# Kernel optimization log

Measured on AMD Instinct MI355X. Metric: run time of the kernel, lower is better.

The kernel has to match this reference:

```python
import jax, jax.numpy as jnp
import numpy as np

N, E, F, HID, HEADS, L, B, R = 50000, 400000, 64, 256, 4, 4, 16, 8
C = HID // HEADS  # per-head channels = 64
LN_EPS = 1e-5
NEG_SLOPE = 0.2  # GATConv LeakyReLU default


def _posenc(n, d):
    pos = jnp.arange(n, dtype=jnp.float32)[:, None]
    i = jnp.arange(d, dtype=jnp.float32)[None, :]
    rates = 1.0 / 10000.0 ** (2.0 * jnp.floor(i / 2.0) / d)
    ang = pos * rates
    return jnp.where(jnp.arange(d)[None, :] % 2 == 0, jnp.sin(ang), jnp.cos(ang))


def _layernorm(x, g, b):
    mu = x.mean(-1, keepdims=True)
    var = ((x - mu) ** 2).mean(-1, keepdims=True)
    return (x - mu) * jax.lax.rsqrt(var + LN_EPS) * g + b


def _gat_layer(x, src, dst, W, a_src, a_dst, bias):
    # x: [N, HID]; W: [HID, HID]; a_src/a_dst: [HEADS, C]; bias: [HID]
    h = (x @ W).reshape(N, HEADS, C)
    s_src = (h * a_src[None]).sum(-1)  # [N, HEADS]
    s_dst = (h * a_dst[None]).sum(-1)  # [N, HEADS]
    e = jax.nn.leaky_relu(s_src[src] + s_dst[dst], NEG_SLOPE)  # [E', HEADS]
    m = jax.ops.segment_max(e, dst, num_segments=N)
    ex = jnp.exp(e - m[dst])
    denom = jax.ops.segment_sum(ex, dst, num_segments=N)
    alpha = ex / denom[dst]  # softmax over incoming edges per dst node
    out = jax.ops.segment_sum(alpha[:, :, None] * h[src], dst, num_segments=N)
    return out.reshape(N, HID) + bias


def setup_inputs() -> dict:
    key = jax.random.key(0)
    ks = jax.random.split(key, 20)
    sc = 0.05
    batch = jnp.sort(jax.random.randint(ks[2], (N,), 0, B))
    return {
        "x": jax.random.normal(ks[0], (N, F), jnp.float32),
        "region_emb_w": jax.random.normal(ks[3], (R, F), jnp.float32) * sc,
        "in_proj_w": jax.random.normal(ks[4], (3 * F, HID), jnp.float32) * sc,
        "in_proj_b": jnp.zeros((HID,), jnp.float32),
        "gat_w": jax.random.normal(ks[5], (L, HID, HID), jnp.float32) * sc,
        "att_src": jax.random.normal(ks[6], (L, HEADS, C), jnp.float32) * sc,
        "att_dst": jax.random.normal(ks[7], (L, HEADS, C), jnp.float32) * sc,
        "gat_b": jnp.zeros((L, HID), jnp.float32),
        "ln_g": jnp.ones((L, HID), jnp.float32),
        "ln_b": jnp.zeros((L, HID), jnp.float32),
        "ro_w1": jax.random.normal(ks[8], (HID, HID), jnp.float32) * sc,
        "ro_b1": jnp.zeros((HID,), jnp.float32),
        "ro_w2": jax.random.normal(ks[9], (HID, HID), jnp.float32) * sc,
        "ro_b2": jnp.zeros((HID,), jnp.float32),
        "edge_index": jax.random.randint(ks[1], (2, E), 0, N),
        "batch": batch,
        "region_ids": jax.random.randint(ks[10], (N,), 0, R),
    }


def reference(x, region_emb_w, in_proj_w, in_proj_b, gat_w, att_src, att_dst,
              gat_b, ln_g, ln_b, ro_w1, ro_b1, ro_w2, ro_b2,
              edge_index, batch, region_ids):
    # input features: x | region embedding | sinusoidal posenc  -> [N, 3F]
    feats = jnp.concatenate([x, region_emb_w[region_ids], _posenc(N, F)], axis=-1)
    h = feats @ in_proj_w + in_proj_b
    # add self loops once (GATConv add_self_loops=True)
    loop = jnp.arange(N)
    src = jnp.concatenate([edge_index[0], loop])
    dst = jnp.concatenate([edge_index[1], loop])
    for l in range(L):
        h = _gat_layer(h, src, dst, gat_w[l], att_src[l], att_dst[l], gat_b[l])
        h = _layernorm(jax.nn.relu(h), ln_g[l], ln_b[l])
        # dropout is identity in eval mode
    # global mean pool over graphs
    sums = jax.ops.segment_sum(h, batch, num_segments=B)
    cnts = jax.ops.segment_sum(jnp.ones((N,), h.dtype), batch, num_segments=B)
    pooled = sums / jnp.maximum(cnts, 1.0)[:, None]  # [B, HID]
    out = jax.nn.gelu(pooled @ ro_w1 + ro_b1, approximate=False) @ ro_w2 + ro_b2
    return out
```

## Files before the change

### kernel.cpp

```cpp
#include <hip/hip_runtime.h>
#include <cmath>

typedef unsigned short u16;
typedef unsigned char u8;
typedef unsigned int u32;
typedef short bf16x8 __attribute__((ext_vector_type(8)));
typedef float f32x4 __attribute__((ext_vector_type(4)));
typedef float f32x2 __attribute__((ext_vector_type(2)));

#define NN 50000
#define MP 50048
#define EE 400000
#define ET 450000
#define HIDD 256
#define KIN 192
#define LN_EPSF 1e-5f

__device__ __forceinline__ float bf2f(u16 u){ return __uint_as_float(((u32)u)<<16); }
__device__ __forceinline__ u16 f2bf(float f){
  u32 x = __float_as_uint(f);
  u32 r = x + 0x7fffu + ((x>>16)&1u);
  return (u16)(r>>16);
}
__device__ __forceinline__ u32 pack2(float a, float b){ return (u32)f2bf(a) | ((u32)f2bf(b)<<16); }
__device__ __forceinline__ u8 f2fp8(float v){
  return (u8)(__builtin_amdgcn_cvt_pk_fp8_f32(v, v, 0, false) & 0xff);
}

__device__ __forceinline__ void dma16(const u16* g, u16* lds){
  __builtin_amdgcn_global_load_lds(
      (const __attribute__((address_space(1))) void*)g,
      (__attribute__((address_space(3))) void*)lds, 16, 0, 0);
}

__global__ __launch_bounds__(256) void k_setup(
    const float* __restrict__ x, const float* __restrict__ remb, const int* __restrict__ rid,
    u16* __restrict__ feats,
    const float* __restrict__ ipw, const float* __restrict__ gatw,
    u16* __restrict__ wtin, u16* __restrict__ wtl,
    const float* __restrict__ asrc, const float* __restrict__ adst, u16* __restrict__ vmat,
    const int* __restrict__ ei, int* __restrict__ deg)
{
  int b = blockIdx.x;
  if (b < 1564){
    int u = b*256 + threadIdx.x;
    int n = u >> 3;
    int c0 = (u & 7) * 8;
    uint4 o = {0u,0u,0u,0u};
    if (n < NN){
      const float* xp = x + (size_t)n*64 + c0;
      float4 v0 = *(const float4*)xp;
      float4 v1 = *(const float4*)(xp + 4);
      o.x = pack2(v0.x, v0.y); o.y = pack2(v0.z, v0.w);
      o.z = pack2(v1.x, v1.y); o.w = pack2(v1.z, v1.w);
    }
    *(uint4*)(feats + (size_t)n*192 + c0) = o;
  } else if (b < 3128){
    int u = (b-1564)*256 + threadIdx.x;
    int n = u >> 3;
    int c0 = (u & 7) * 8;
    uint4 o = {0u,0u,0u,0u};
    if (n < NN){
      const float* rp = remb + (size_t)rid[n]*64 + c0;
      float4 v0 = *(const float4*)rp;
      float4 v1 = *(const float4*)(rp + 4);
      o.x = pack2(v0.x, v0.y); o.y = pack2(v0.z, v0.w);
      o.z = pack2(v1.x, v1.y); o.w = pack2(v1.z, v1.w);
    }
    *(uint4*)(feats + (size_t)n*192 + 64 + c0) = o;
  } else if (b < 4692){
    int u = (b-3128)*256 + threadIdx.x;
    int n = u >> 3;
    int i0 = (u & 7) * 8;
    uint4 o = {0u,0u,0u,0u};
    if (n < NN){
      float fn = (float)n;
      float os[8];
      #pragma unroll
      for (int m=0;m<4;++m){
        float rate = exp2f(-(float)(i0 + 2*m) * (1.0f/64.0f) * 13.287712379549449f);
        float s, c;
        __sincosf(fn * rate, &s, &c);
        os[2*m] = s; os[2*m+1] = c;
      }
      o.x = pack2(os[0], os[1]); o.y = pack2(os[2], os[3]);
      o.z = pack2(os[4], os[5]); o.w = pack2(os[6], os[7]);
    }
    *(uint4*)(feats + (size_t)n*192 + 128 + i0) = o;
  } else if (b < 5908){
    int idx = (b - 4692)*256 + threadIdx.x;
    if (idx < 49152){
      int n = idx / 192, k = idx - n*192;
      wtin[idx] = f2bf(ipw[k*256 + n]);
    } else {
      int j = idx - 49152;
      if (j < 262144){
        int l = j >> 16, rem = j & 65535;
        int n = rem >> 8, k = rem & 255;
        wtl[j] = f2bf(gatw[l*65536 + k*256 + n]);
      }
    }
  } else if (b < 5972){
    int idx = (b - 5908)*256 + threadIdx.x;
    if (idx < 16384){
      int l = idx >> 12, rem = idx & 4095, v = rem >> 8, k = rem & 255;
      float s = 0.f;
      if (v < 8){
        const float* a = (v < 4) ? (asrc + l*256 + v*64) : (adst + l*256 + (v-4)*64);
        const float* w = gatw + (size_t)l*65536 + k*256 + (v & 3)*64;
        #pragma unroll 8
        for (int c=0;c<64;++c) s += w[c]*a[c];
      }
      vmat[idx] = f2bf(s);
    }
  } else {
    int i = (b - 5972)*256 + threadIdx.x;
    if (i < ET){
      int d = (i < EE) ? ei[EE + i] : (i - EE);
      atomicAdd(&deg[d], 1);
    }
  }
}

__global__ void k_scan1(const int* __restrict__ deg, int* __restrict__ row_off, int* __restrict__ part){
  __shared__ int s[256];
  int n = blockIdx.x*256 + threadIdx.x;
  int v = (n < NN) ? deg[n] : 0;
  s[threadIdx.x] = v;
  __syncthreads();
  for (int off=1; off<256; off<<=1){
    int t = (threadIdx.x >= off) ? s[threadIdx.x - off] : 0;
    __syncthreads();
    s[threadIdx.x] += t;
    __syncthreads();
  }
  if (n < NN) row_off[n] = s[threadIdx.x] - v;
  if (threadIdx.x == 255) part[blockIdx.x] = s[255];
}

__global__ void k_scan23(int* __restrict__ row_off, const int* __restrict__ part, int nparts){
  __shared__ int sp[256];
  int t = threadIdx.x;
  sp[t] = (t < nparts && t < (int)blockIdx.x) ? part[t] : 0;
  __syncthreads();
  for (int off=128; off; off>>=1){
    if (t < off) sp[t] += sp[t+off];
    __syncthreads();
  }
  int n = blockIdx.x*256 + t;
  if (n < NN) row_off[n] += sp[0];
}

__global__ void k_scatter(const int* __restrict__ ei, const int* __restrict__ row_off,
                          int* __restrict__ cur, int* __restrict__ csr_src){
  int i = blockIdx.x*blockDim.x + threadIdx.x;
  if (i >= ET) return;
  int s, d;
  if (i < EE){ s = ei[i]; d = ei[EE + i]; } else { s = i - EE; d = i - EE; }
  int pos = row_off[d] + atomicAdd(&cur[d], 1);
  csr_src[pos] = s;
}

template<int K>
__global__ __launch_bounds__(256, 3) void k_gemm(
    const u16* __restrict__ A, const u16* __restrict__ Wt,
    const float* __restrict__ bias, const u16* __restrict__ vmat,
    float* __restrict__ ss, float* __restrict__ sd,
    u16* __restrict__ C, u8* __restrict__ C8, int M)
{
  __shared__ u16 Asl[2][128*32];
  __shared__ u16 Bsl[2][128*32];
  int tid = threadIdx.x;
  int wave = tid >> 6, lane = tid & 63, quad = lane >> 4, lm = lane & 15;

  int bid0 = blockIdx.x;
  int xcd = bid0 & 7, off = bid0 >> 3;
  const int q = 782 >> 3, r = 782 & 7;
  int wgid = (xcd < r ? xcd*(q+1) : r*(q+1) + (xcd - r)*q) + off;
  int r0 = (wgid >> 1) * 128;
  int cb = wgid & 1;

  int rW = (wave >> 1) * 64;
  int cW = (wave & 1) * 64;
  bool doScore = vmat && (cb == 0) && ((wave & 1) == 0);

  f32x4 acc[4][4] = {};
  f32x4 accs[4] = {};

  auto stage = [&](int buf, int k0){
    for (int m = wave; m < 8; m += 4){
      int s = m*64 + lane;
      int rr = s >> 2, p = s & 3;
      int c = p ^ ((rr >> 2) & 3);
      dma16(A + (size_t)(r0 + rr)*K + k0 + c*8, &Asl[buf][m*512]);
    }
    for (int m = wave; m < 8; m += 4){
      int s = m*64 + lane;
      int rr = s >> 2, p = s & 3;
      int c = p ^ ((rr >> 2) & 3);
      dma16(Wt + (size_t)(cb*128 + rr)*K + k0 + c*8, &Bsl[buf][m*512]);
    }
  };

  stage(0, 0);
  __syncthreads();

  for (int ks = 0; ks < K/32; ++ks){
    int cur = ks & 1;
    if (ks + 1 < K/32) stage(cur ^ 1, (ks+1)*32);

    bf16x8 a[4], b[4];
    #pragma unroll
    for (int i=0;i<4;++i){
      int row = rW + i*16 + lm;
      int slot = row*4 + (quad ^ ((row >> 2) & 3));
      a[i] = *(const bf16x8*)(&Asl[cur][slot*8]);
    }
    #pragma unroll
    for (int j=0;j<4;++j){
      int row = cW + j*16 + lm;
      int slot = row*4 + (quad ^ ((row >> 2) & 3));
      b[j] = *(const bf16x8*)(&Bsl[cur][slot*8]);
    }
    #pragma unroll
    for (int i=0;i<4;++i)
      #pragma unroll
      for (int j=0;j<4;++j)
        acc[i][j] = __builtin_amdgcn_mfma_f32_16x16x32_bf16(a[i], b[j], acc[i][j], 0, 0, 0);
    if (doScore){
      bf16x8 bs = *(const bf16x8*)(vmat + (size_t)lm*K + ks*32 + quad*8);
      #pragma unroll
      for (int i=0;i<4;++i)
        accs[i] = __builtin_amdgcn_mfma_f32_16x16x32_bf16(a[i], bs, accs[i], 0, 0, 0);
    }
    __syncthreads();
  }

  if (doScore){
    #pragma unroll
    for (int i=0;i<4;++i){
      #pragma unroll
      for (int r2=0;r2<4;++r2){
        int row = r0 + rW + i*16 + quad*4 + r2;
        if (row < M){
          if (lm < 4)      ss[row*4 + lm]     = accs[i][r2];
          else if (lm < 8) sd[row*4 + lm - 4] = accs[i][r2];
        }
      }
    }
  }

  #pragma unroll
  for (int i=0;i<4;++i){
    #pragma unroll
    for (int r2=0;r2<4;++r2){
      int row = r0 + rW + i*16 + quad*4 + r2;
      if (row < M){
        #pragma unroll
        for (int j=0;j<4;++j){
          int col = cb*128 + cW + j*16 + lm;
          float v = acc[i][j][r2];
          if (bias) v += bias[col];
          if (C)  C[(size_t)row*256 + col] = f2bf(v);
          if (C8) C8[(size_t)row*256 + col] = f2fp8(v);
        }
      }
    }
  }
}

__global__ __launch_bounds__(256) void k_aggregate(
    const u8* __restrict__ h8, const float* __restrict__ ssrc, const float* __restrict__ sdst,
    const int* __restrict__ row_off, const int* __restrict__ deg, const int* __restrict__ csr_src,
    const float* __restrict__ bias, const float* __restrict__ g, const float* __restrict__ bb,
    u16* __restrict__ hout, u8* __restrict__ hout8)
{
  int wv = (blockIdx.x*blockDim.x + threadIdx.x) >> 6;
  int lane = threadIdx.x & 63;
  int half = lane >> 5;
  int hl = lane & 31;
  int n = wv*2 + half;
  if (n >= NN) return;
  int c0 = hl*8;
  int head = hl >> 3;
  float sdh = sdst[n*4 + head];
  int ro = row_off[n];
  int dg = deg[n];
  float denA = 0.f, denB = 0.f;
  float a0=0,a1=0,a2=0,a3=0,a4=0,a5=0,a6=0,a7=0;
  float b0=0,b1=0,b2=0,b3=0,b4=0,b5=0,b6=0,b7=0;

  int sA = csr_src[ro];
  int sB = (1 < dg) ? csr_src[ro + 1] : 0;
  uint2 uA = *(const uint2*)(h8 + (size_t)sA*HIDD + c0);
  uint2 uB = *(const uint2*)(h8 + (size_t)sB*HIDD + c0);
  float fA = ssrc[sA*4 + head];
  float fB = ssrc[sB*4 + head];

  for (int j = 0; j < dg; j += 2){
    bool hasB = (j + 1 < dg);
    int nA = (j + 2 < dg) ? csr_src[ro + j + 2] : 0;
    int nB = (j + 3 < dg) ? csr_src[ro + j + 3] : 0;
    uint2 vA = *(const uint2*)(h8 + (size_t)nA*HIDD + c0);
    uint2 vB = *(const uint2*)(h8 + (size_t)nB*HIDD + c0);
    float gA = ssrc[nA*4 + head];
    float gB = ssrc[nB*4 + head];

    float eA = fA + sdh;
    eA = (eA > 0.f) ? eA : 0.2f*eA;
    float xA = __expf(eA);
    denA += xA;
    f32x2 pA0 = __builtin_amdgcn_cvt_pk_f32_fp8((int)uA.x, false);
    f32x2 pA1 = __builtin_amdgcn_cvt_pk_f32_fp8((int)uA.x, true);
    f32x2 pA2 = __builtin_amdgcn_cvt_pk_f32_fp8((int)uA.y, false);
    f32x2 pA3 = __builtin_amdgcn_cvt_pk_f32_fp8((int)uA.y, true);
    a0 += xA*pA0.x; a1 += xA*pA0.y; a2 += xA*pA1.x; a3 += xA*pA1.y;
    a4 += xA*pA2.x; a5 += xA*pA2.y; a6 += xA*pA3.x; a7 += xA*pA3.y;
    if (hasB){
      float eB = fB + sdh;
      eB = (eB > 0.f) ? eB : 0.2f*eB;
      float xB = __expf(eB);
      denB += xB;
      f32x2 pB0 = __builtin_amdgcn_cvt_pk_f32_fp8((int)uB.x, false);
      f32x2 pB1 = __builtin_amdgcn_cvt_pk_f32_fp8((int)uB.x, true);
      f32x2 pB2 = __builtin_amdgcn_cvt_pk_f32_fp8((int)uB.y, false);
      f32x2 pB3 = __builtin_amdgcn_cvt_pk_f32_fp8((int)uB.y, true);
      b0 += xB*pB0.x; b1 += xB*pB0.y; b2 += xB*pB1.x; b3 += xB*pB1.y;
      b4 += xB*pB2.x; b5 += xB*pB2.y; b6 += xB*pB3.x; b7 += xB*pB3.y;
    }
    sA = nA; sB = nB; uA = vA; uB = vB; fA = gA; fB = gB;
  }

  float inv = 1.f / (denA + denB);
  float y[8];
  y[0]=a0+b0; y[1]=a1+b1; y[2]=a2+b2; y[3]=a3+b3;
  y[4]=a4+b4; y[5]=a5+b5; y[6]=a6+b6; y[7]=a7+b7;
  float4 bi0 = *(const float4*)(bias + c0);
  float4 bi1 = *(const float4*)(bias + c0 + 4);
  y[0]=fmaxf(y[0]*inv+bi0.x,0.f); y[1]=fmaxf(y[1]*inv+bi0.y,0.f);
  y[2]=fmaxf(y[2]*inv+bi0.z,0.f); y[3]=fmaxf(y[3]*inv+bi0.w,0.f);
  y[4]=fmaxf(y[4]*inv+bi1.x,0.f); y[5]=fmaxf(y[5]*inv+bi1.y,0.f);
  y[6]=fmaxf(y[6]*inv+bi1.z,0.f); y[7]=fmaxf(y[7]*inv+bi1.w,0.f);
  float sum = (y[0]+y[1])+(y[2]+y[3])+((y[4]+y[5])+(y[6]+y[7]));
  #pragma unroll
  for (int o=16;o>=1;o>>=1) sum += __shfl_xor(sum, o);
  float mu = sum * (1.f/256.f);
  float d[8], sq = 0.f;
  #pragma unroll
  for (int k=0;k<8;++k){ d[k] = y[k]-mu; sq += d[k]*d[k]; }
  #pragma unroll
  for (int o=16;o>=1;o>>=1) sq += __shfl_xor(sq, o);
  float rs = rsqrtf(sq*(1.f/256.f) + LN_EPSF);
  float4 g0 = *(const float4*)(g + c0);
  float4 g1 = *(const float4*)(g + c0 + 4);
  float4 q0 = *(const float4*)(bb + c0);
  float4 q1 = *(const float4*)(bb + c0 + 4);
  float o0 = d[0]*rs*g0.x + q0.x, o1 = d[1]*rs*g0.y + q0.y;
  float o2 = d[2]*rs*g0.z + q0.z, o3 = d[3]*rs*g0.w + q0.w;
  float o4v= d[4]*rs*g1.x + q1.x, o5 = d[5]*rs*g1.y + q1.y;
  float o6 = d[6]*rs*g1.z + q1.z, o7 = d[7]*rs*g1.w + q1.w;
  if (hout8){
    u32 w0 = (u32)__builtin_amdgcn_cvt_pk_fp8_f32(o0, o1, 0, false);
    w0 = (u32)__builtin_amdgcn_cvt_pk_fp8_f32(o2, o3, (int)w0, true);
    u32 w1 = (u32)__builtin_amdgcn_cvt_pk_fp8_f32(o4v, o5, 0, false);
    w1 = (u32)__builtin_amdgcn_cvt_pk_fp8_f32(o6, o7, (int)w1, true);
    uint2 o8; o8.x = w0; o8.y = w1;
    *(uint2*)(hout8 + (size_t)n*HIDD + c0) = o8;
  } else {
    uint4 o4;
    o4.x = pack2(o0, o1);
    o4.y = pack2(o2, o3);
    o4.z = pack2(o4v, o5);
    o4.w = pack2(o6, o7);
    *(uint4*)(hout + (size_t)n*HIDD + c0) = o4;
  }
}

__global__ __launch_bounds__(256) void k_pool(
    const u8* __restrict__ h8, const int* __restrict__ batch,
    float* __restrict__ pooled, float* __restrict__ cnt)
{
  const int chunk = 50;
  int t = threadIdx.x;
  int n0 = blockIdx.x*chunk;
  int n1 = min(n0 + chunk, NN);
  if (n0 >= n1) return;
  float acc = 0.f;
  int curb = batch[n0];
  int runStart = n0;
  bool hi = (t & 2) != 0;
  for (int n=n0; n<n1; ++n){
    int b = batch[n];
    if (b != curb){
      atomicAdd(&pooled[curb*HIDD + t], acc);
      if (t == 0) atomicAdd(&cnt[curb], (float)(n - runStart));
      acc = 0.f; curb = b; runStart = n;
    }
    u32 w = *(const u32*)(h8 + (size_t)n*HIDD + (t & ~3));
    f32x2 p = hi ? __builtin_amdgcn_cvt_pk_f32_fp8((int)w, true)
                 : __builtin_amdgcn_cvt_pk_f32_fp8((int)w, false);
    acc += (t & 1) ? p.y : p.x;
  }
  atomicAdd(&pooled[curb*HIDD + t], acc);
  if (t == 0) atomicAdd(&cnt[curb], (float)(n1 - runStart));
}

__global__ __launch_bounds__(256) void k_readout(
    const float* __restrict__ pooled, const float* __restrict__ cnt,
    const float* __restrict__ w1, const float* __restrict__ b1,
    const float* __restrict__ w2, const float* __restrict__ b2,
    float* __restrict__ out)
{
  __shared__ float p[256], mid[256];
  int b = blockIdx.x, t = threadIdx.x;
  float c = fmaxf(cnt[b], 1.f);
  p[t] = pooled[b*HIDD + t] / c;
  __syncthreads();
  float acc = b1[t];
  for (int k=0;k<256;++k) acc += p[k]*w1[k*256+t];
  mid[t] = 0.5f*acc*(1.f + erff(acc*0.70710678118654752f));
  __syncthreads();
  float acc2 = b2[t];
  for (int k=0;k<256;++k) acc2 += mid[k]*w2[k*256+t];
  out[b*HIDD + t] = acc2;
}

extern "C" void kernel_launch(void* const* d_in, const int* in_sizes, int n_in,
                              void* d_out, int out_size, void* d_ws, size_t ws_size,
                              hipStream_t stream)
{
  const float* x    = (const float*)d_in[0];
  const float* remb = (const float*)d_in[1];
  const float* ipw  = (const float*)d_in[2];
  const float* ipb  = (const float*)d_in[3];
  const float* gatw = (const float*)d_in[4];
  const float* asrc = (const float*)d_in[5];
  const float* adst = (const float*)d_in[6];
  const float* gatb = (const float*)d_in[7];
  const float* lng  = (const float*)d_in[8];
  const float* lnb  = (const float*)d_in[9];
  const float* row1 = (const float*)d_in[10];
  const float* rob1 = (const float*)d_in[11];
  const float* row2 = (const float*)d_in[12];
  const float* rob2 = (const float*)d_in[13];
  const int* ei   = (const int*)d_in[14];
  const int* batch= (const int*)d_in[15];
  const int* rid  = (const int*)d_in[16];

  char* ws = (char*)d_ws;
  int*   deg  = (int*)  (ws + 0);
  int*   cur  = (int*)  (ws + 200192);
  float* cnt  = (float*)(ws + 400384);
  float* pool = (float*)(ws + 400640);
  int*   row  = (int*)  (ws + 417024);
  int*   part = (int*)  (ws + 617216);
  int*   csr  = (int*)  (ws + 618240);
  float* ss   = (float*)(ws + 2418432);
  float* sd   = (float*)(ws + 3219200);
  u16*   vmat = (u16*)  (ws + 4019968);
  u16*   feats= (u16*)  (ws + 4052736);
  u16*   wtin = (u16*)  (ws + 23271168);
  u16*   wtl  = (u16*)  (ws + 23369472);
  u16*   hA   = (u16*)  (ws + 23893760);
  u8*    hA8  = (u8*)   (ws + 23893760);
  u8*    hB8  = (u8*)   (ws + 49518336);

  (void)hipMemsetAsync(ws, 0, 417024, stream);

  k_setup <<<7730, 256, 0, stream>>>(x, remb, rid, feats, ipw, gatw, wtin, wtl,
                                     asrc, adst, vmat, ei, deg);
  k_scan1 <<<196, 256, 0, stream>>>(deg, row, part);
  k_scan23<<<196, 256, 0, stream>>>(row, part, 196);
  k_scatter<<<1758, 256, 0, stream>>>(ei, row, cur, csr);

  k_gemm<KIN><<<782, 256, 0, stream>>>(feats, wtin, ipb, nullptr,
                                       nullptr, nullptr, hA, nullptr, NN);

  for (int l = 0; l < 4; ++l){
    k_gemm<HIDD><<<782, 256, 0, stream>>>(hA, wtl + (size_t)l*HIDD*HIDD, nullptr,
                                          vmat + (size_t)l*16*256, ss, sd,
                                          nullptr, hB8, NN);
    if (l < 3){
      k_aggregate<<<6250, 256, 0, stream>>>(hB8, ss, sd, row, deg, csr,
                                            gatb + l*HIDD, lng + l*HIDD, lnb + l*HIDD,
                                            hA, nullptr);
    } else {
      k_aggregate<<<6250, 256, 0, stream>>>(hB8, ss, sd, row, deg, csr,
                                            gatb + l*HIDD, lng + l*HIDD, lnb + l*HIDD,
                                            nullptr, hA8);
    }
  }

  k_pool   <<<1000, 256, 0, stream>>>(hA8, batch, pool, cnt);
  k_readout<<<16, 256, 0, stream>>>(pool, cnt, row1, rob1, row2, rob2, (float*)d_out);
}
```

Baseline: 452.9 us.

## Fold input projection into first GAT layer weight, dropping one GEMM pass

Precomputes the product of the input projection weight and the first GAT layer weight, plus the folded bias and attention-score vectors, inside the setup kernel. The first layer then runs a single K=192 GEMM straight from the raw features to the fp8 hidden buffer and scores, instead of a K=192 GEMM followed by a K=256 GEMM. This removes one full 50000x256 GEMM and its bf16 intermediate write and read. In exchange, setup does a serial 256-long dot product per output element, and folding the weights in fp32 before rounding to bf16 changes numerics slightly.

```diff
diff --git a/kernel.cpp b/kernel.cpp
--- a/kernel.cpp
+++ b/kernel.cpp
@@ -39,7 +39,8 @@
     const float* __restrict__ ipw, const float* __restrict__ gatw,
     u16* __restrict__ wtin, u16* __restrict__ wtl,
     const float* __restrict__ asrc, const float* __restrict__ adst, u16* __restrict__ vmat,
-    const int* __restrict__ ei, int* __restrict__ deg)
+    const int* __restrict__ ei, int* __restrict__ deg,
+    const float* __restrict__ ipb, u16* __restrict__ vmatc, float* __restrict__ bias0)
 {
   int b = blockIdx.x;
   if (b < 1564){
@@ -90,8 +91,12 @@
   } else if (b < 5908){
     int idx = (b - 4692)*256 + threadIdx.x;
     if (idx < 49152){
-      int n = idx / 192, k = idx - n*192;
-      wtin[idx] = f2bf(ipw[k*256 + n]);
+      int k = idx >> 8, n = idx & 255;
+      const float* wrow = ipw + (size_t)k*256;
+      float s = 0.f;
+      #pragma unroll 8
+      for (int j=0;j<256;++j) s += wrow[j] * gatw[(size_t)j*256 + n];
+      wtin[n*192 + k] = f2bf(s);
     } else {
       int j = idx - 49152;
       if (j < 262144){
@@ -113,8 +118,45 @@
       }
       vmat[idx] = f2bf(s);
     }
+  } else if (b < 5980){
+    int v = b - 5972;
+    __shared__ float w0a[256];
+    int t = threadIdx.x;
+    {
+      const float* a = (v < 4) ? (asrc + v*64) : (adst + (v-4)*64);
+      const float* w = gatw + (size_t)t*256 + (v & 3)*64;
+      float s = 0.f;
+      #pragma unroll 8
+      for (int c=0;c<64;++c) s += w[c]*a[c];
+      w0a[t] = s;
+    }
+    __syncthreads();
+    if (t < 192){
+      const float* wrow = ipw + (size_t)t*256;
+      float s = 0.f;
+      #pragma unroll 8
+      for (int j=0;j<256;++j) s += wrow[j]*w0a[j];
+      vmatc[v*192 + t] = f2bf(s);
+      vmatc[(v+8)*192 + t] = 0;
+    }
+  } else if (b < 5981){
+    int t = threadIdx.x;
+    __shared__ float c0[256];
+    {
+      float s = 0.f;
+      for (int k=0;k<256;++k) s += ipb[k] * gatw[(size_t)k*256 + t];
+      c0[t] = s;
+      bias0[t] = s;
+    }
+    __syncthreads();
+    if (t < 8){
+      const float* a = (t < 4) ? (asrc + t*64) : (adst + (t-4)*64);
+      float s = 0.f;
+      for (int c=0;c<64;++c) s += c0[(t & 3)*64 + c] * a[c];
+      bias0[256 + t] = s;
+    }
   } else {
-    int i = (b - 5972)*256 + threadIdx.x;
+    int i = (b - 5981)*256 + threadIdx.x;
     if (i < ET){
       int d = (i < EE) ? ei[EE + i] : (i - EE);
       atomicAdd(&deg[d], 1);
@@ -165,6 +207,7 @@
 __global__ __launch_bounds__(256, 3) void k_gemm(
     const u16* __restrict__ A, const u16* __restrict__ Wt,
     const float* __restrict__ bias, const u16* __restrict__ vmat,
+    const float* __restrict__ sbias,
     float* __restrict__ ss, float* __restrict__ sd,
     u16* __restrict__ C, u8* __restrict__ C8, int M)
 {
@@ -237,14 +280,16 @@
   }
 
   if (doScore){
+    float sb = sbias ? sbias[lm & 7] : 0.f;
     #pragma unroll
     for (int i=0;i<4;++i){
       #pragma unroll
       for (int r2=0;r2<4;++r2){
         int row = r0 + rW + i*16 + quad*4 + r2;
         if (row < M){
-          if (lm < 4)      ss[row*4 + lm]     = accs[i][r2];
-          else if (lm < 8) sd[row*4 + lm - 4] = accs[i][r2];
+          float sv = accs[i][r2] + sb;
+          if (lm < 4)      ss[row*4 + lm]     = sv;
+          else if (lm < 8) sd[row*4 + lm - 4] = sv;
         }
       }
     }
@@ -464,22 +509,27 @@
   u16*   hA   = (u16*)  (ws + 23893760);
   u8*    hA8  = (u8*)   (ws + 23893760);
   u8*    hB8  = (u8*)   (ws + 49518336);
+  u16*   vmatc= (u16*)  (ws + 62330624);
+  float* bias0= (float*)(ws + 62336768);
 
   (void)hipMemsetAsync(ws, 0, 417024, stream);
 
-  k_setup <<<7730, 256, 0, stream>>>(x, remb, rid, feats, ipw, gatw, wtin, wtl,
-                                     asrc, adst, vmat, ei, deg);
+  k_setup <<<7739, 256, 0, stream>>>(x, remb, rid, feats, ipw, gatw, wtin, wtl,
+                                     asrc, adst, vmat, ei, deg, ipb, vmatc, bias0);
   k_scan1 <<<196, 256, 0, stream>>>(deg, row, part);
   k_scan23<<<196, 256, 0, stream>>>(row, part, 196);
   k_scatter<<<1758, 256, 0, stream>>>(ei, row, cur, csr);
 
-  k_gemm<KIN><<<782, 256, 0, stream>>>(feats, wtin, ipb, nullptr,
-                                       nullptr, nullptr, hA, nullptr, NN);
-
-  for (int l = 0; l < 4; ++l){
+  k_gemm<KIN><<<782, 256, 0, stream>>>(feats, wtin, bias0, vmatc, bias0 + 256,
+                                       ss, sd, nullptr, hB8, NN);
+  k_aggregate<<<6250, 256, 0, stream>>>(hB8, ss, sd, row, deg, csr,
+                                        gatb + 0*HIDD, lng + 0*HIDD, lnb + 0*HIDD,
+                                        hA, nullptr);
+
+  for (int l = 1; l < 4; ++l){
     k_gemm<HIDD><<<782, 256, 0, stream>>>(hA, wtl + (size_t)l*HIDD*HIDD, nullptr,
-                                          vmat + (size_t)l*16*256, ss, sd,
-                                          nullptr, hB8, NN);
+                                          vmat + (size_t)l*16*256, nullptr,
+                                          ss, sd, nullptr, hB8, NN);
     if (l < 3){
       k_aggregate<<<6250, 256, 0, stream>>>(hB8, ss, sd, row, deg, csr,
                                             gatb + l*HIDD, lng + l*HIDD, lnb + l*HIDD,
```

Measured after the change: 440.7 us. -2.7%, faster.
